# Optimization experiments

Measured on AMD Instinct MI355X. Metric: run time of the kernel, lower is better.

The kernel has to match this reference:

```python
import jax, jax.numpy as jnp
import numpy as np


def conv1d(x, w, b, pad):
    # x: [B, C, L], w: [O, C, K], torch nn.Conv1d semantics (cross-correlation + bias)
    y = jax.lax.conv_general_dilated(
        x, w, window_strides=(1,), padding=[(pad, pad)],
        dimension_numbers=("NCH", "OIH", "NCH"))
    return y + b[None, :, None]


def setup_inputs() -> dict:
    key = jax.random.key(0)
    ks = jax.random.split(key, 11)
    B, C, L = 32, 4, 65536
    def rn(k, shape, fan_in):
        # kaiming-ish scale so activations stay sane
        return jax.random.normal(k, shape, dtype=jnp.float32) / np.sqrt(fan_in)
    return {
        "x": jax.random.normal(ks[0], (B, C, L), dtype=jnp.float32),
        "w_motif": rn(ks[1], (40, 4, 51), 4 * 51),
        "b_motif": jnp.zeros((40,), jnp.float32),
        "w_reduce": rn(ks[2], (4, 40, 1), 40),
        "b_reduce": jnp.zeros((4,), jnp.float32),
        "w_fft": rn(ks[3], (4, 4, 401), 4 * 401),
        "b_fft": jnp.zeros((4,), jnp.float32),
        "w_expand": rn(ks[4], (40, 4, 1), 4),
        "b_expand": jnp.zeros((40,), jnp.float32),
        "w_effect": rn(ks[5], (2, 40, 601), 40 * 601),
        "b_effect": jnp.zeros((2,), jnp.float32),
    }


def reference(x, w_motif, b_motif, w_reduce, b_reduce, w_fft, b_fft,
              w_expand, b_expand, w_effect, b_effect):
    # motif layer + softplus
    y = jax.nn.softplus(conv1d(x, w_motif, b_motif, 25))          # [B,40,L]
    # synergy: factorized FFT-conv block (reduce 1x1 -> long conv -> expand 1x1)
    s = conv1d(y, w_reduce, b_reduce, 0)                          # [B,4,L]
    s = conv1d(s, w_fft, b_fft, 200)                              # [B,4,L]
    s = conv1d(s, w_expand, b_expand, 0)                          # [B,40,L]
    motifact = jax.nn.sigmoid(s) * y                              # gated
    # effect: long conv -> sigmoid
    y_pred = jax.nn.sigmoid(conv1d(motifact, w_effect, b_effect, 300))  # [B,2,L]
    return y_pred[:, :, 500:-500]
```

## Files before the change

kernel.cpp:

```cpp
#include <hip/hip_runtime.h>
#include <hip/hip_bf16.h>
#include <math.h>

#define LEN 65536
#define LOUT 64536
typedef __hip_bfloat16 bf16;
typedef __attribute__((ext_vector_type(8))) short short8;
typedef __attribute__((ext_vector_type(4))) float f32x4;

__device__ inline float b2f(bf16 h) { return __bfloat162float(h); }
__device__ inline bf16 f2b(float f) { return __float2bfloat16(f); }
__device__ inline float us2f(unsigned short u) { bf16 h = *(bf16*)&u; return __bfloat162float(h); }
__device__ inline float softplus_f(float v) {
    return fmaxf(v, 0.f) + __logf(1.f + __expf(-fabsf(v)));
}

__global__ __launch_bounds__(256) void k_x2b(const float* __restrict__ x,
                                             short* __restrict__ xb, int n8) {
    int i = blockIdx.x * 256 + threadIdx.x;
    if (i >= n8) return;
    const float* src = x + (size_t)i * 8;
    float4 f0 = *(const float4*)src;
    float4 f1 = *(const float4*)(src + 4);
    short8 v; bf16 h;
    h = f2b(f0.x); v[0] = *(short*)&h;
    h = f2b(f0.y); v[1] = *(short*)&h;
    h = f2b(f0.z); v[2] = *(short*)&h;
    h = f2b(f0.w); v[3] = *(short*)&h;
    h = f2b(f1.x); v[4] = *(short*)&h;
    h = f2b(f1.y); v[5] = *(short*)&h;
    h = f2b(f1.z); v[6] = *(short*)&h;
    h = f2b(f1.w); v[7] = *(short*)&h;
    *(short8*)(xb + (size_t)i * 8) = v;
}

__global__ __launch_bounds__(256) void k_prep_mot(const float* __restrict__ w_motif,
                                                  short* __restrict__ fragA) {
    int idx = blockIdx.x * 256 + threadIdx.x;
    if (idx >= 40 * 4 * 3 * 64 * 8) return;
    int i = idx & 7;
    int lane = (idx >> 3) & 63;
    int rest = idx >> 9;
    int qc = rest % 3; rest /= 3;
    int c = rest & 3; int o = rest >> 2;
    int dlt = lane & 15, kb = lane >> 4;
    int m = 32 * qc + 8 * kb + i;
    int k = m - 7 - dlt;
    float v = (k >= 0 && k < 51) ? w_motif[(o * 4 + c) * 51 + k] : 0.f;
    bf16 h = f2b(v);
    fragA[idx] = *(short*)&h;
}

#define MOT_BLKS 522
#define MOT_PAD  528
__global__ __launch_bounds__(256, 2) void k_motif_mfma(const short* __restrict__ xb,
        const short* __restrict__ fragA, const float* __restrict__ b_motif,
        const float* __restrict__ w_reduce, const float* __restrict__ b_reduce,
        bf16* __restrict__ y, bf16* __restrict__ s1, int b0) {
    __shared__ __align__(16) short bwin[4][MOT_PAD * 8];
    const int tid = threadIdx.x;
    const int lane = tid & 63, wv = tid >> 6;
    const int wg = blockIdx.x, bl = blockIdx.y;
    const int bg = b0 + bl;
    const int L0 = wg * 4096;
    const int win0 = L0 - 32;
    const int ln15 = lane & 15, lkb = lane >> 4;

    #pragma unroll 1
    for (int c = 0; c < 4; ++c) {
        const short* src = xb + ((size_t)bg * 4 + c) * LEN;
        for (int Lb = tid; Lb < MOT_BLKS; Lb += 256) {
            int gi = win0 + Lb * 8;
            short8 v;
            if (gi >= 0 && gi + 8 <= LEN) {
                v = *(const short8*)(src + gi);
            } else {
                #pragma unroll
                for (int j = 0; j < 8; ++j)
                    v[j] = (gi + j >= 0 && gi + j < LEN) ? src[gi + j] : (short)0;
            }
            int Pb = Lb ^ ((Lb >> 3) & 7);
            *(short8*)(&bwin[c][Pb * 8]) = v;
        }
    }
    __syncthreads();

    float s1a[4][4][4];
    #pragma unroll
    for (int nt = 0; nt < 4; ++nt)
        #pragma unroll
        for (int c = 0; c < 4; ++c) {
            float bc = b_reduce[c];
            #pragma unroll
            for (int j = 0; j < 4; ++j) s1a[nt][c][j] = bc;
        }

    #pragma unroll 1
    for (int og = 0; og < 10; ++og) {
        f32x4 acc[4][4];
        #pragma unroll
        for (int Mt = 0; Mt < 4; ++Mt)
            #pragma unroll
            for (int nt = 0; nt < 4; ++nt)
                acc[Mt][nt] = (f32x4){0.f, 0.f, 0.f, 0.f};

        #pragma unroll 1
        for (int c = 0; c < 4; ++c) {
            short8 afc[4][3];
            #pragma unroll
            for (int Mt = 0; Mt < 4; ++Mt)
                #pragma unroll
                for (int qc = 0; qc < 3; ++qc)
                    afc[Mt][qc] = *(const short8*)(fragA +
                        (size_t)(((og * 4 + Mt) * 12 + c * 3 + qc) * 64 + lane) * 8);
            #pragma unroll
            for (int nt = 0; nt < 4; ++nt) {
                const int tt = wv * 4 + nt;
                #pragma unroll
                for (int qc = 0; qc < 3; ++qc) {
                    int L = 32 * tt + 2 * ln15 + 4 * qc + lkb;
                    int P = L ^ ((L >> 3) & 7);
                    short8 bfr = *(const short8*)(&bwin[c][P * 8]);
                    #pragma unroll
                    for (int Mt = 0; Mt < 4; ++Mt)
                        acc[Mt][nt] = __builtin_amdgcn_mfma_f32_16x16x32_bf16(
                            afc[Mt][qc], bfr, acc[Mt][nt], 0, 0, 0);
                }
            }
        }

        #pragma unroll
        for (int Mt = 0; Mt < 4; ++Mt) {
            const int o = og * 4 + Mt;
            const float bb = b_motif[o];
            const float wr0 = w_reduce[0 * 40 + o], wr1 = w_reduce[1 * 40 + o];
            const float wr2 = w_reduce[2 * 40 + o], wr3 = w_reduce[3 * 40 + o];
            #pragma unroll
            for (int nt = 0; nt < 4; ++nt) {
                int tt = wv * 4 + nt;
                int pos = L0 + tt * 256 + 16 * ln15 + 4 * lkb;
                float v0 = softplus_f(acc[Mt][nt][0] + bb);
                float v1 = softplus_f(acc[Mt][nt][1] + bb);
                float v2 = softplus_f(acc[Mt][nt][2] + bb);
                float v3 = softplus_f(acc[Mt][nt][3] + bb);
                ushort4 st; bf16 h;
                h = f2b(v0); st.x = *(unsigned short*)&h;
                h = f2b(v1); st.y = *(unsigned short*)&h;
                h = f2b(v2); st.z = *(unsigned short*)&h;
                h = f2b(v3); st.w = *(unsigned short*)&h;
                *(ushort4*)(&y[((size_t)bl * 40 + o) * LEN + pos]) = st;
                s1a[nt][0][0] += wr0 * v0; s1a[nt][0][1] += wr0 * v1;
                s1a[nt][0][2] += wr0 * v2; s1a[nt][0][3] += wr0 * v3;
                s1a[nt][1][0] += wr1 * v0; s1a[nt][1][1] += wr1 * v1;
                s1a[nt][1][2] += wr1 * v2; s1a[nt][1][3] += wr1 * v3;
                s1a[nt][2][0] += wr2 * v0; s1a[nt][2][1] += wr2 * v1;
                s1a[nt][2][2] += wr2 * v2; s1a[nt][2][3] += wr2 * v3;
                s1a[nt][3][0] += wr3 * v0; s1a[nt][3][1] += wr3 * v1;
                s1a[nt][3][2] += wr3 * v2; s1a[nt][3][3] += wr3 * v3;
            }
        }
    }

    #pragma unroll
    for (int nt = 0; nt < 4; ++nt) {
        int tt = wv * 4 + nt;
        int pos = L0 + tt * 256 + 16 * ln15 + 4 * lkb;
        #pragma unroll
        for (int c = 0; c < 4; ++c) {
            ushort4 st; bf16 h;
            h = f2b(s1a[nt][c][0]); st.x = *(unsigned short*)&h;
            h = f2b(s1a[nt][c][1]); st.y = *(unsigned short*)&h;
            h = f2b(s1a[nt][c][2]); st.z = *(unsigned short*)&h;
            h = f2b(s1a[nt][c][3]); st.w = *(unsigned short*)&h;
            *(ushort4*)(&s1[((size_t)bl * 4 + c) * LEN + pos]) = st;
        }
    }
}

__global__ __launch_bounds__(256) void k_prep_fft(const float* __restrict__ w_fft,
                                                  short* __restrict__ fragA) {
    int idx = blockIdx.x * 256 + threadIdx.x;
    if (idx >= 4 * 7 * 4 * 2 * 64 * 8) return;
    int i = idx & 7;
    int lane = (idx >> 3) & 63;
    int rest = idx >> 9;
    int ql = rest & 1; rest >>= 1;
    int Mt = rest & 3; rest >>= 2;
    int qb = rest % 7; int c = rest / 7;
    int dlt = lane & 15, kb = lane >> 4;
    int kkp = 32 * (qb * 2 + ql) + 8 * kb + i;
    int kk = kkp - dlt;
    float v = (kk >= 0 && kk < 401) ? w_fft[(Mt * 4 + c) * 401 + kk] : 0.f;
    bf16 h = f2b(v);
    fragA[idx] = *(short*)&h;
}

#define FFT_BLKS 568
__global__ __launch_bounds__(256) void k_fft(const short* __restrict__ s1,
        const short* __restrict__ fragA, const float* __restrict__ b_fft,
        bf16* __restrict__ s2) {
    __shared__ __align__(16) short bwin[4][FFT_BLKS * 8];
    const int tid = threadIdx.x;
    const int lane = tid & 63, wv = tid >> 6;
    const int wg = blockIdx.x, bl = blockIdx.y;
    const int P0 = wg * 4096;
    const int win0 = P0 - 200;
    const int ln15 = lane & 15, lkb = lane >> 4;

    f32x4 acc[4][4];
    #pragma unroll
    for (int Mt = 0; Mt < 4; ++Mt)
        #pragma unroll
        for (int nt = 0; nt < 4; ++nt)
            acc[Mt][nt] = (f32x4){0.f, 0.f, 0.f, 0.f};

    #pragma unroll 1
    for (int cl = 0; cl < 4; ++cl) {
        const short* src = s1 + ((size_t)bl * 4 + cl) * LEN;
        for (int Lb = tid; Lb < FFT_BLKS; Lb += 256) {
            int gi = win0 + Lb * 8;
            short8 v;
            if (gi >= 0 && gi + 8 <= LEN) {
                v = *(const short8*)(src + gi);
            } else {
                #pragma unroll
                for (int j = 0; j < 8; ++j)
                    v[j] = (gi + j >= 0 && gi + j < LEN) ? src[gi + j] : (short)0;
            }
            int Pb = Lb ^ ((Lb >> 3) & 7);
            *(short8*)(&bwin[cl][Pb * 8]) = v;
        }
    }
    __syncthreads();

    #pragma unroll 1
    for (int cl = 0; cl < 4; ++cl) {
        #pragma unroll 1
        for (int qb = 0; qb < 7; ++qb) {
            short8 af[4][2];
            #pragma unroll
            for (int Mt = 0; Mt < 4; ++Mt)
                #pragma unroll
                for (int ql = 0; ql < 2; ++ql)
                    af[Mt][ql] = *(const short8*)(fragA +
                        (size_t)((((cl * 7 + qb) * 4 + Mt) * 2 + ql) * 64 + lane) * 8);
            #pragma unroll
            for (int nt = 0; nt < 4; ++nt) {
                const int tt = wv * 4 + nt;
                #pragma unroll
                for (int ql = 0; ql < 2; ++ql) {
                    int qc = qb * 2 + ql;
                    int L = 2 * ln15 + lkb + 4 * qc + 32 * tt;
                    int P = L ^ ((L >> 3) & 7);
                    short8 bfr = *(const short8*)(&bwin[cl][P * 8]);
                    #pragma unroll
                    for (int Mt = 0; Mt < 4; ++Mt)
                        acc[Mt][nt] = __builtin_amdgcn_mfma_f32_16x16x32_bf16(
                            af[Mt][ql], bfr, acc[Mt][nt], 0, 0, 0);
                }
            }
        }
    }

    #pragma unroll
    for (int Mt = 0; Mt < 4; ++Mt) {
        float bb = b_fft[Mt];
        #pragma unroll
        for (int nt = 0; nt < 4; ++nt) {
            int tt = wv * 4 + nt;
            int pos = P0 + tt * 256 + 16 * ln15 + 4 * lkb;
            ushort4 st; bf16 h;
            h = f2b(acc[Mt][nt][0] + bb); st.x = *(unsigned short*)&h;
            h = f2b(acc[Mt][nt][1] + bb); st.y = *(unsigned short*)&h;
            h = f2b(acc[Mt][nt][2] + bb); st.z = *(unsigned short*)&h;
            h = f2b(acc[Mt][nt][3] + bb); st.w = *(unsigned short*)&h;
            *(ushort4*)(&s2[((size_t)bl * 4 + Mt) * LEN + pos]) = st;
        }
    }
}

__global__ __launch_bounds__(256) void k_prep(const float* __restrict__ w_eff,
                                              short* __restrict__ fragA) {
    int idx = blockIdx.x * 256 + threadIdx.x;
    if (idx >= 40 * 20 * 4 * 64 * 8) return;
    int i = idx & 7;
    int lane = (idx >> 3) & 63;
    int rest = idx >> 9;
    int Mt = rest & 3; rest >>= 2;
    int ks = rest % 20; int c = rest / 20;
    int row16 = lane & 15, kb = lane >> 4;
    int dlt = 16 * (Mt & 1) + row16;
    int o = Mt >> 1;
    int kp = 32 * ks + 8 * kb + i;
    int kk = kp - dlt;
    float v = (kk >= 0 && kk < 601) ? w_eff[(o * 40 + c) * 601 + kk] : 0.f;
    bf16 h = __float2bfloat16(v);
    fragA[idx] = *(short*)&h;
}

#define EFF_NBLK 336
#define EFF_SH (EFF_NBLK * 8)
__device__ __forceinline__ void eff_prefetch(const short* __restrict__ mact,
        size_t chanBase, int cc, int tid, int win0, short8 (&yreg)[2][4]) {
    #pragma unroll
    for (int it = 0; it < 2; ++it) {
        int Lb = tid + it * 256;
        if (Lb < EFF_NBLK) {
            int gi = win0 + Lb * 8;
            bool full = (gi + 8 <= LEN);
            #pragma unroll
            for (int ch = 0; ch < 4; ++ch) {
                const short* src = mact + (chanBase + cc * 4 + ch) * (size_t)LEN;
                short8 v = {0, 0, 0, 0, 0, 0, 0, 0};
                if (full) {
                    v = *(const short8*)(src + gi);
                } else {
                    #pragma unroll
                    for (int j = 0; j < 8; ++j)
                        v[j] = (gi + j < LEN) ? src[gi + j] : (short)0;
                }
                yreg[it][ch] = v;
            }
        }
    }
}

__global__ __launch_bounds__(256, 3) void k_effect(const short* __restrict__ mact,
        const short* __restrict__ s2,
        const short* __restrict__ fragA,
        const float* __restrict__ w_expand, const float* __restrict__ b_expand,
        float* __restrict__ part) {
    __shared__ __align__(16) char smem[2 * EFF_SH * 4 * 2 + 160 * 4 + 40 * 4];
    short (*bwin)[EFF_SH]  = (short(*)[EFF_SH])smem;
    short (*s2win)[EFF_SH] = (short(*)[EFF_SH])(smem + EFF_SH * 4 * 2);
    float* wexp = (float*)(smem + 2 * EFF_SH * 4 * 2);
    float* bexp = wexp + 160;
    float* red  = (float*)smem;

    const int tid = threadIdx.x;
    const int lane = tid & 63, wv = tid >> 6;
    const int wgl = blockIdx.x, bl = blockIdx.y, half = blockIdx.z;
    const int coff = half * 20;
    const int L0 = wgl * 2048;
    const int win0 = L0 + 200;
    const int ln15 = lane & 15, lkb = lane >> 4;
    const size_t chanBase = (size_t)bl * 40 + coff;

    if (tid < 160) wexp[tid] = w_expand[tid];
    if (tid < 40) bexp[tid] = b_expand[tid];
    #pragma unroll 1
    for (int c = 0; c < 4; ++c) {
        const short* sp = s2 + ((size_t)bl * 4 + c) * LEN;
        for (int Lb = tid; Lb < EFF_NBLK; Lb += 256) {
            int gi = win0 + Lb * 8;
            short8 v = {0, 0, 0, 0, 0, 0, 0, 0};
            if (gi + 8 <= LEN) {
                v = *(const short8*)(sp + gi);
            } else {
                #pragma unroll
                for (int j = 0; j < 8; ++j)
                    v[j] = (gi + j < LEN) ? sp[gi + j] : (short)0;
            }
            *(short8*)(&s2win[c][Lb * 8]) = v;
        }
    }

    f32x4 acc[4][4];
    #pragma unroll
    for (int Mt = 0; Mt < 4; ++Mt)
        #pragma unroll
        for (int nt = 0; nt < 4; ++nt)
            acc[Mt][nt] = (f32x4){0.f, 0.f, 0.f, 0.f};

    short8 yreg[2][4];
    eff_prefetch(mact, chanBase, 0, tid, win0, yreg);

    #pragma unroll 1
    for (int cc = 0; cc < 5; ++cc) {
        __syncthreads();
        #pragma unroll
        for (int it = 0; it < 2; ++it) {
            int Lb = tid + it * 256;
            if (Lb < EFF_NBLK) {
                float s2v[4][8];
                #pragma unroll
                for (int c = 0; c < 4; ++c) {
                    short8 sv = *(const short8*)(&s2win[c][Lb * 8]);
                    #pragma unroll
                    for (int j = 0; j < 8; ++j) s2v[c][j] = us2f((unsigned short)sv[j]);
                }
                int P = Lb ^ ((Lb >> 3) & 7);
                #pragma unroll
                for (int ch = 0; ch < 4; ++ch) {
                    int o = coff + cc * 4 + ch;
                    float w0 = wexp[o * 4 + 0], w1 = wexp[o * 4 + 1];
                    float w2 = wexp[o * 4 + 2], w3 = wexp[o * 4 + 3];
                    float be = bexp[o];
                    short8 w;
                    #pragma unroll
                    for (int j = 0; j < 8; ++j) {
                        float sg = be + w0 * s2v[0][j] + w1 * s2v[1][j]
                                      + w2 * s2v[2][j] + w3 * s2v[3][j];
                        float g = __builtin_amdgcn_rcpf(1.f + __expf(-sg));
                        float yv = us2f((unsigned short)yreg[it][ch][j]) * g;
                        bf16 h = f2b(yv);
                        w[j] = *(short*)&h;
                    }
                    *(short8*)(&bwin[ch][P * 8]) = w;
                }
            }
        }
        __syncthreads();
        if (cc < 4) eff_prefetch(mact, chanBase, cc + 1, tid, win0, yreg);
        const int cg = coff + cc * 4 + wv;
        #pragma unroll 1
        for (int ks = 0; ks < 20; ++ks) {
            short8 af[4];
            #pragma unroll
            for (int Mt = 0; Mt < 4; ++Mt)
                af[Mt] = *(const short8*)(fragA +
                    (size_t)(((cg * 20 + ks) * 4 + Mt) * 64 + lane) * 8);
            #pragma unroll
            for (int nt = 0; nt < 4; ++nt) {
                int L = 64 * nt + 4 * ln15 + 4 * ks + lkb;
                int P = L ^ ((L >> 3) & 7);
                short8 bfr = *(const short8*)(&bwin[wv][P * 8]);
                #pragma unroll
                for (int Mt = 0; Mt < 4; ++Mt)
                    acc[Mt][nt] = __builtin_amdgcn_mfma_f32_16x16x32_bf16(
                        af[Mt], bfr, acc[Mt][nt], 0, 0, 0);
            }
        }
    }

    __syncthreads();
    if (wv == 1 || wv == 3) {
        float* p = red + (wv >> 1) * 4096;
        #pragma unroll
        for (int Mt = 0; Mt < 4; ++Mt)
            #pragma unroll
            for (int nt = 0; nt < 4; ++nt)
                *(f32x4*)(p + (Mt * 4 + nt) * 256 + lane * 4) = acc[Mt][nt];
    }
    __syncthreads();
    if (wv == 0 || wv == 2) {
        float* p = red + (wv >> 1) * 4096;
        #pragma unroll
        for (int Mt = 0; Mt < 4; ++Mt)
            #pragma unroll
            for (int nt = 0; nt < 4; ++nt)
                acc[Mt][nt] += *(const f32x4*)(p + (Mt * 4 + nt) * 256 + lane * 4);
    }
    __syncthreads();
    if (wv == 2) {
        #pragma unroll
        for (int Mt = 0; Mt < 4; ++Mt)
            #pragma unroll
            for (int nt = 0; nt < 4; ++nt)
                *(f32x4*)(red + (Mt * 4 + nt) * 256 + lane * 4) = acc[Mt][nt];
    }
    __syncthreads();
    if (wv == 0) {
        #pragma unroll
        for (int Mt = 0; Mt < 4; ++Mt) {
            const int o = Mt >> 1;
            #pragma unroll
            for (int nt = 0; nt < 4; ++nt) {
                f32x4 a = acc[Mt][nt];
                a += *(const f32x4*)(red + (Mt * 4 + nt) * 256 + lane * 4);
                int pos = L0 + 512 * nt + 32 * ln15 + 16 * (Mt & 1) + 4 * lkb;
                float4 st; st.x = a[0]; st.y = a[1]; st.z = a[2]; st.w = a[3];
                *(float4*)(&part[(((size_t)bl * 2 + half) * 2 + o) * LEN + pos]) = st;
            }
        }
    }
}

__global__ __launch_bounds__(256) void k_comb(const float* __restrict__ part,
        const float* __restrict__ b_eff, float* __restrict__ out, int b0) {
    const int tid = threadIdx.x;
    const int bl = blockIdx.y, bg = b0 + bl;
    int l4 = (blockIdx.x * 256 + tid) * 4;
    if (l4 >= LOUT) return;
    #pragma unroll
    for (int Mt = 0; Mt < 2; ++Mt) {
        float bb = b_eff[Mt];
        float4 p0 = *(const float4*)(&part[(((size_t)bl * 2 + 0) * 2 + Mt) * LEN + l4]);
        float4 p1 = *(const float4*)(&part[(((size_t)bl * 2 + 1) * 2 + Mt) * LEN + l4]);
        float4 st;
        st.x = __builtin_amdgcn_rcpf(1.f + __expf(-(p0.x + p1.x + bb)));
        st.y = __builtin_amdgcn_rcpf(1.f + __expf(-(p0.y + p1.y + bb)));
        st.z = __builtin_amdgcn_rcpf(1.f + __expf(-(p0.z + p1.z + bb)));
        st.w = __builtin_amdgcn_rcpf(1.f + __expf(-(p0.w + p1.w + bb)));
        *(float4*)(&out[((size_t)bg * 2 + Mt) * LOUT + l4]) = st;
    }
}

extern "C" void kernel_launch(void* const* d_in, const int* in_sizes, int n_in,
                              void* d_out, int out_size, void* d_ws, size_t ws_size,
                              hipStream_t stream) {
    const float* x        = (const float*)d_in[0];
    const float* w_motif  = (const float*)d_in[1];
    const float* b_motif  = (const float*)d_in[2];
    const float* w_reduce = (const float*)d_in[3];
    const float* b_reduce = (const float*)d_in[4];
    const float* w_fft    = (const float*)d_in[5];
    const float* b_fft    = (const float*)d_in[6];
    const float* w_expand = (const float*)d_in[7];
    const float* b_expand = (const float*)d_in[8];
    const float* w_eff    = (const float*)d_in[9];
    const float* b_eff    = (const float*)d_in[10];
    float* out = (float*)d_out;

    const size_t FRAGA_EFF = (size_t)40 * 20 * 4 * 64 * 8 * 2;
    const size_t FRAGA_FFT = (size_t)4 * 7 * 4 * 2 * 64 * 8 * 2;
    const size_t FRAGA_MOT = (size_t)40 * 4 * 3 * 64 * 8 * 2;
    const size_t XB_B      = (size_t)32 * 4 * LEN * 2;
    const size_t HEAD = FRAGA_EFF + FRAGA_FFT + FRAGA_MOT + XB_B;

    short* fragA_eff = (short*)d_ws;
    short* fragA_fft = (short*)((char*)d_ws + FRAGA_EFF);
    short* fragA_mot = (short*)((char*)d_ws + FRAGA_EFF + FRAGA_FFT);
    short* xb        = (short*)((char*)d_ws + FRAGA_EFF + FRAGA_FFT + FRAGA_MOT);
    char*  rest      = (char*)d_ws + HEAD;

    const size_t PB_Y = (size_t)40 * LEN * 2;
    const size_t PB_S = (size_t)4 * LEN * 2;
    const size_t PERB = PB_Y + 2 * PB_S + (size_t)2 * 2 * LEN * 4;
    size_t avail = (ws_size > HEAD) ? (ws_size - HEAD) : 0;
    int nb = (int)(avail / PERB);
    if (nb > 32) nb = 32;
    if (nb < 1) nb = 1;

    bf16*  y    = (bf16*)rest;
    bf16*  s1   = (bf16*)(rest + PB_Y * (size_t)nb);
    bf16*  s2   = (bf16*)(rest + (PB_Y + PB_S) * (size_t)nb);
    float* part = (float*)(rest + (PB_Y + 2 * PB_S) * (size_t)nb);

    hipLaunchKernelGGL(k_prep,     dim3(6400), dim3(256), 0, stream, w_eff, fragA_eff);
    hipLaunchKernelGGL(k_prep_fft, dim3(448),  dim3(256), 0, stream, w_fft, fragA_fft);
    hipLaunchKernelGGL(k_prep_mot, dim3(960),  dim3(256), 0, stream, w_motif, fragA_mot);
    hipLaunchKernelGGL(k_x2b,      dim3(4096), dim3(256), 0, stream, x, xb,
                       (int)(32 * 4 * LEN / 8));

    for (int b0 = 0; b0 < 32; b0 += nb) {
        int nbb = (32 - b0 < nb) ? (32 - b0) : nb;
        hipLaunchKernelGGL(k_motif_mfma, dim3(16, nbb), dim3(256), 0, stream,
                           xb, fragA_mot, b_motif, w_reduce, b_reduce, y, s1, b0);
        hipLaunchKernelGGL(k_fft, dim3(16, nbb), dim3(256), 0, stream,
                           (const short*)s1, fragA_fft, b_fft, s2);
        hipLaunchKernelGGL(k_effect, dim3(32, nbb, 2), dim3(256), 0, stream,
                           (const short*)y, (const short*)s2, fragA_eff,
                           w_expand, b_expand, part);
        hipLaunchKernelGGL(k_comb, dim3(64, nbb), dim3(256), 0, stream,
                           part, b_eff, out, b0);
    }
}
```

Measured before the change: 395.0 us.

## Switch effect conv to 32x32x16 MFMA with halved Toeplitz weight fragments

Rewrites the effect-conv inner loop to use 32x32x16 bf16 MFMA instead of 16x16x32. The banded Toeplitz A fragments are repacked with 16-wide diagonal offsets, which halves the fragA buffer and the prep grid. The A fragment is now software-prefetched one step ahead, and the LDS XOR swizzle on the B window is dropped. This reduces zero-padded MAC work and global fragment loads, but the unswizzled LDS reads may cause bank conflicts, and the loop runs twice as many iterations.

```diff
diff --git a/kernel.cpp b/kernel.cpp
--- a/kernel.cpp
+++ b/kernel.cpp
@@ -7,6 +7,7 @@
 typedef __hip_bfloat16 bf16;
 typedef __attribute__((ext_vector_type(8))) short short8;
 typedef __attribute__((ext_vector_type(4))) float f32x4;
+typedef __attribute__((ext_vector_type(16))) float f32x16;
 
 __device__ inline float b2f(bf16 h) { return __bfloat162float(h); }
 __device__ inline bf16 f2b(float f) { return __float2bfloat16(f); }
@@ -282,16 +283,14 @@
 __global__ __launch_bounds__(256) void k_prep(const float* __restrict__ w_eff,
                                               short* __restrict__ fragA) {
     int idx = blockIdx.x * 256 + threadIdx.x;
-    if (idx >= 40 * 20 * 4 * 64 * 8) return;
+    if (idx >= 40 * 40 * 64 * 8) return;
     int i = idx & 7;
     int lane = (idx >> 3) & 63;
     int rest = idx >> 9;
-    int Mt = rest & 3; rest >>= 2;
-    int ks = rest % 20; int c = rest / 20;
-    int row16 = lane & 15, kb = lane >> 4;
-    int dlt = 16 * (Mt & 1) + row16;
-    int o = Mt >> 1;
-    int kp = 32 * ks + 8 * kb + i;
+    int ks = rest % 40; int c = rest / 40;
+    int row = lane & 31, hi = lane >> 5;
+    int o = row >> 4, dlt = row & 15;
+    int kp = 16 * ks + 8 * hi + i;
     int kk = kp - dlt;
     float v = (kk >= 0 && kk < 601) ? w_eff[(o * 40 + c) * 601 + kk] : 0.f;
     bf16 h = __float2bfloat16(v);
@@ -339,11 +338,11 @@
 
     const int tid = threadIdx.x;
     const int lane = tid & 63, wv = tid >> 6;
+    const int ln31 = lane & 31, lhi = lane >> 5;
     const int wgl = blockIdx.x, bl = blockIdx.y, half = blockIdx.z;
     const int coff = half * 20;
     const int L0 = wgl * 2048;
     const int win0 = L0 + 200;
-    const int ln15 = lane & 15, lkb = lane >> 4;
     const size_t chanBase = (size_t)bl * 40 + coff;
 
     if (tid < 160) wexp[tid] = w_expand[tid];
@@ -365,12 +364,12 @@
         }
     }
 
-    f32x4 acc[4][4];
-    #pragma unroll
-    for (int Mt = 0; Mt < 4; ++Mt)
-        #pragma unroll
-        for (int nt = 0; nt < 4; ++nt)
-            acc[Mt][nt] = (f32x4){0.f, 0.f, 0.f, 0.f};
+    f32x16 acc[4];
+    #pragma unroll
+    for (int tt = 0; tt < 4; ++tt)
+        #pragma unroll
+        for (int j = 0; j < 16; ++j)
+            acc[tt][j] = 0.f;
 
     short8 yreg[2][4];
     eff_prefetch(mact, chanBase, 0, tid, win0, yreg);
@@ -389,7 +388,6 @@
                     #pragma unroll
                     for (int j = 0; j < 8; ++j) s2v[c][j] = us2f((unsigned short)sv[j]);
                 }
-                int P = Lb ^ ((Lb >> 3) & 7);
                 #pragma unroll
                 for (int ch = 0; ch < 4; ++ch) {
                     int o = coff + cc * 4 + ch;
@@ -406,30 +404,27 @@
                         bf16 h = f2b(yv);
                         w[j] = *(short*)&h;
                     }
-                    *(short8*)(&bwin[ch][P * 8]) = w;
+                    *(short8*)(&bwin[ch][Lb * 8]) = w;
                 }
             }
         }
         __syncthreads();
         if (cc < 4) eff_prefetch(mact, chanBase, cc + 1, tid, win0, yreg);
         const int cg = coff + cc * 4 + wv;
+        const short* bw = bwin[wv];
+        const int bofs = 2 * ln31 + lhi;
+        short8 afc = *(const short8*)(fragA + (size_t)((cg * 40 + 0) * 64 + lane) * 8);
         #pragma unroll 1
-        for (int ks = 0; ks < 20; ++ks) {
-            short8 af[4];
-            #pragma unroll
-            for (int Mt = 0; Mt < 4; ++Mt)
-                af[Mt] = *(const short8*)(fragA +
-                    (size_t)(((cg * 20 + ks) * 4 + Mt) * 64 + lane) * 8);
-            #pragma unroll
-            for (int nt = 0; nt < 4; ++nt) {
-                int L = 64 * nt + 4 * ln15 + 4 * ks + lkb;
-                int P = L ^ ((L >> 3) & 7);
-                short8 bfr = *(const short8*)(&bwin[wv][P * 8]);
-                #pragma unroll
-                for (int Mt = 0; Mt < 4; ++Mt)
-                    acc[Mt][nt] = __builtin_amdgcn_mfma_f32_16x16x32_bf16(
-                        af[Mt], bfr, acc[Mt][nt], 0, 0, 0);
-            }
+        for (int ks = 0; ks < 40; ++ks) {
+            short8 afn;
+            if (ks < 39)
+                afn = *(const short8*)(fragA + (size_t)((cg * 40 + ks + 1) * 64 + lane) * 8);
+            #pragma unroll
+            for (int tt = 0; tt < 4; ++tt) {
+                short8 bfr = *(const short8*)(&bw[(64 * tt + 2 * ks + bofs) * 8]);
+                acc[tt] = __builtin_amdgcn_mfma_f32_32x32x16_bf16(afc, bfr, acc[tt], 0, 0, 0);
+            }
+            afc = afn;
         }
     }
 
@@ -437,39 +432,51 @@
     if (wv == 1 || wv == 3) {
         float* p = red + (wv >> 1) * 4096;
         #pragma unroll
-        for (int Mt = 0; Mt < 4; ++Mt)
-            #pragma unroll
-            for (int nt = 0; nt < 4; ++nt)
-                *(f32x4*)(p + (Mt * 4 + nt) * 256 + lane * 4) = acc[Mt][nt];
+        for (int tt = 0; tt < 4; ++tt)
+            #pragma unroll
+            for (int g = 0; g < 4; ++g) {
+                float4 v4 = {acc[tt][4 * g + 0], acc[tt][4 * g + 1],
+                             acc[tt][4 * g + 2], acc[tt][4 * g + 3]};
+                *(float4*)(p + (tt * 4 + g) * 256 + lane * 4) = v4;
+            }
     }
     __syncthreads();
     if (wv == 0 || wv == 2) {
         float* p = red + (wv >> 1) * 4096;
         #pragma unroll
-        for (int Mt = 0; Mt < 4; ++Mt)
-            #pragma unroll
-            for (int nt = 0; nt < 4; ++nt)
-                acc[Mt][nt] += *(const f32x4*)(p + (Mt * 4 + nt) * 256 + lane * 4);
+        for (int tt = 0; tt < 4; ++tt)
+            #pragma unroll
+            for (int g = 0; g < 4; ++g) {
+                float4 v4 = *(const float4*)(p + (tt * 4 + g) * 256 + lane * 4);
+                acc[tt][4 * g + 0] += v4.x; acc[tt][4 * g + 1] += v4.y;
+                acc[tt][4 * g + 2] += v4.z; acc[tt][4 * g + 3] += v4.w;
+            }
     }
     __syncthreads();
     if (wv == 2) {
         #pragma unroll
-        for (int Mt = 0; Mt < 4; ++Mt)
-            #pragma unroll
-            for (int nt = 0; nt < 4; ++nt)
-                *(f32x4*)(red + (Mt * 4 + nt) * 256 + lane * 4) = acc[Mt][nt];
+        for (int tt = 0; tt < 4; ++tt)
+            #pragma unroll
+            for (int g = 0; g < 4; ++g) {
+                float4 v4 = {acc[tt][4 * g + 0], acc[tt][4 * g + 1],
+                             acc[tt][4 * g + 2], acc[tt][4 * g + 3]};
+                *(float4*)(red + (tt * 4 + g) * 256 + lane * 4) = v4;
+            }
     }
     __syncthreads();
     if (wv == 0) {
         #pragma unroll
-        for (int Mt = 0; Mt < 4; ++Mt) {
-            const int o = Mt >> 1;
-            #pragma unroll
-            for (int nt = 0; nt < 4; ++nt) {
-                f32x4 a = acc[Mt][nt];
-                a += *(const f32x4*)(red + (Mt * 4 + nt) * 256 + lane * 4);
-                int pos = L0 + 512 * nt + 32 * ln15 + 16 * (Mt & 1) + 4 * lkb;
-                float4 st; st.x = a[0]; st.y = a[1]; st.z = a[2]; st.w = a[3];
+        for (int tt = 0; tt < 4; ++tt) {
+            #pragma unroll
+            for (int g = 0; g < 4; ++g) {
+                float4 v4 = *(const float4*)(red + (tt * 4 + g) * 256 + lane * 4);
+                float4 st;
+                st.x = acc[tt][4 * g + 0] + v4.x;
+                st.y = acc[tt][4 * g + 1] + v4.y;
+                st.z = acc[tt][4 * g + 2] + v4.z;
+                st.w = acc[tt][4 * g + 3] + v4.w;
+                int o = g >> 1;
+                int pos = L0 + 512 * tt + 16 * ln31 + 8 * (g & 1) + 4 * lhi;
                 *(float4*)(&part[(((size_t)bl * 2 + half) * 2 + o) * LEN + pos]) = st;
             }
         }
@@ -512,7 +519,7 @@
     const float* b_eff    = (const float*)d_in[10];
     float* out = (float*)d_out;
 
-    const size_t FRAGA_EFF = (size_t)40 * 20 * 4 * 64 * 8 * 2;
+    const size_t FRAGA_EFF = (size_t)40 * 40 * 64 * 8 * 2;
     const size_t FRAGA_FFT = (size_t)4 * 7 * 4 * 2 * 64 * 8 * 2;
     const size_t FRAGA_MOT = (size_t)40 * 4 * 3 * 64 * 8 * 2;
     const size_t XB_B      = (size_t)32 * 4 * LEN * 2;
@@ -537,7 +544,7 @@
     bf16*  s2   = (bf16*)(rest + (PB_Y + PB_S) * (size_t)nb);
     float* part = (float*)(rest + (PB_Y + 2 * PB_S) * (size_t)nb);
 
-    hipLaunchKernelGGL(k_prep,     dim3(6400), dim3(256), 0, stream, w_eff, fragA_eff);
+    hipLaunchKernelGGL(k_prep,     dim3(3200), dim3(256), 0, stream, w_eff, fragA_eff);
     hipLaunchKernelGGL(k_prep_fft, dim3(448),  dim3(256), 0, stream, w_fft, fragA_fft);
     hipLaunchKernelGGL(k_prep_mot, dim3(960),  dim3(256), 0, stream, w_motif, fragA_mot);
     hipLaunchKernelGGL(k_x2b,      dim3(4096), dim3(256), 0, stream, x, xb,
```

Measured after the change: 439.6 us. 11.3% more time.
